# Kernel optimization log

Measured on AMD Instinct MI355X. Metric: run time of the kernel, lower is better.

Reference implementation:

```python
import jax, jax.numpy as jnp
import numpy as np

N_NODES = 40000
N_EDGES = 640000
IN_DIM, H_DIM, OUT_DIM = 128, 128, 64


def setup_inputs() -> dict:
    key = jax.random.key(0)
    ks = jax.random.split(key, 16)
    x = jax.random.normal(ks[0], (N_NODES, IN_DIM), dtype=jnp.float32)
    edge_index = jax.random.randint(ks[1], (2, N_EDGES), 0, N_NODES, dtype=jnp.int64)
    dims = [(IN_DIM, H_DIM), (H_DIM, H_DIM), (H_DIM, OUT_DIM)]
    inp = {"x": x, "edge_index": edge_index}
    for l, (di, do) in enumerate(dims):
        s = 1.0 / np.sqrt(di)
        inp[f"Wr{l}"] = jax.random.uniform(ks[2 + 3 * l], (di, do), jnp.float32, -s, s)  # lin_rel weight
        inp[f"br{l}"] = jax.random.uniform(ks[3 + 3 * l], (do,), jnp.float32, -s, s)     # lin_rel bias
        inp[f"Ws{l}"] = jax.random.uniform(ks[4 + 3 * l], (di, do), jnp.float32, -s, s)  # lin_root weight (no bias)
    return inp


def _graph_conv(x, src, dst, Wr, br, Ws):
    # PyG GraphConv (aggr='add'): out = lin_rel(sum_{j in N(i)} x_j) + lin_root(x_i)
    agg = jax.ops.segment_sum(x[src], dst, num_segments=N_NODES)  # [N, d_in]
    return agg @ Wr + br + x @ Ws


def reference(x, edge_index, Wr0, br0, Ws0, Wr1, br1, Ws1, Wr2, br2, Ws2):
    src, dst = edge_index[0], edge_index[1]
    h = x
    for Wr, br, Ws in ((Wr0, br0, Ws0), (Wr1, br1, Ws1), (Wr2, br2, Ws2)):
        h = _graph_conv(h, src, dst, Wr, br, Ws)
        h = jax.nn.relu(h)
        # dropout p=0 / eval mode -> identity
    return jax.nn.log_softmax(h, axis=1)
```

## Files before the change

kernel.cpp:

```cpp
#include <hip/hip_runtime.h>
#include <hip/hip_bf16.h>


#define N_NODES 40000
#define N_EDGES 640000
#define PAD_NODES 40064
#define DEG_CAP   40960
#define ROW_CAP   64

typedef float v4f __attribute__((ext_vector_type(4)));
typedef float v2f __attribute__((ext_vector_type(2)));
typedef short short8 __attribute__((ext_vector_type(8)));

__device__ inline unsigned short f2b(float f) {
    unsigned u = __float_as_uint(f);
    return (unsigned short)((u + 0x7fffu + ((u >> 16) & 1u)) >> 16);
}

__device__ inline unsigned b2f8(unsigned short us) {
    unsigned s  = ((unsigned)us >> 8) & 0x80u;
    unsigned mag = us & 0x7fffu;
    unsigned e8 = mag >> 7, m7 = mag & 0x7fu;
    unsigned out;
    if (e8 < 121u) out = 0u;
    else if (e8 > 135u) out = 0x7eu;
    else {
        unsigned e4 = e8 - 120u;
        unsigned r  = (m7 + 7u + ((m7 >> 4) & 1u)) >> 4;
        if (r == 8u) { r = 0u; e4++; }
        out = (e4 > 15u || (e4 == 15u && r > 6u)) ? 0x7eu : ((e4 << 3) | r);
    }
    return s | out;
}

__device__ inline unsigned pack4_fp8(float f0, float f1, float f2, float f3) {
#if __has_builtin(__builtin_amdgcn_cvt_pk_fp8_f32)
    int w = __builtin_amdgcn_cvt_pk_fp8_f32(f0, f1, 0, false);
    w = __builtin_amdgcn_cvt_pk_fp8_f32(f2, f3, w, true);
    return (unsigned)w;
#else
    return b2f8(f2b(f0)) | (b2f8(f2b(f1)) << 8) |
           (b2f8(f2b(f2)) << 16) | (b2f8(f2b(f3)) << 24);
#endif
}

#if __has_builtin(__builtin_amdgcn_cvt_f32_fp8)
#define F8TOF(w, sel) __builtin_amdgcn_cvt_f32_fp8((int)(w), (sel))
#else
__device__ inline float f8tof_(unsigned b) {
    unsigned e = (b >> 3) & 15u;
    unsigned bits = ((b & 0x80u) << 24) |
                    (e ? (((e + 120u) << 23) | ((b & 7u) << 20)) : 0u);
    return __uint_as_float(bits);
}
#define F8TOF(w, sel) f8tof_(((unsigned)(w) >> ((sel) * 8)) & 0xffu)
#endif

__device__ inline void addp(v2f* a, uint4 q) {
    v2f t0 = { __uint_as_float(q.x << 16), __uint_as_float(q.x & 0xffff0000u) };
    v2f t1 = { __uint_as_float(q.y << 16), __uint_as_float(q.y & 0xffff0000u) };
    v2f t2 = { __uint_as_float(q.z << 16), __uint_as_float(q.z & 0xffff0000u) };
    v2f t3 = { __uint_as_float(q.w << 16), __uint_as_float(q.w & 0xffff0000u) };
    a[0] += t0; a[1] += t1; a[2] += t2; a[3] += t3;
}
__device__ inline void addp8w(v2f* a, unsigned w) {
    v2f t0 = { F8TOF(w, 0), F8TOF(w, 1) };
    v2f t1 = { F8TOF(w, 2), F8TOF(w, 3) };
    a[0] += t0; a[1] += t1;
}
__device__ inline void addp16(v2f* a, uint4 q) {
    addp8w(a + 0, q.x); addp8w(a + 2, q.y);
    addp8w(a + 4, q.z); addp8w(a + 6, q.w);
}

__global__ __launch_bounds__(256) void prep_kernel(const float* __restrict__ Wr0, const float* __restrict__ Ws0,
                                                   const float* __restrict__ Wr1, const float* __restrict__ Ws1,
                                                   const float* __restrict__ Wr2, const float* __restrict__ Ws2,
                                                   const float* __restrict__ x,
                                                   unsigned short* __restrict__ Wt0,
                                                   unsigned short* __restrict__ Wt1,
                                                   unsigned short* __restrict__ Wt2,
                                                   unsigned short* __restrict__ Xb,
                                                   int* __restrict__ deg) {
    int tid = blockIdx.x * 256 + threadIdx.x;
    if (tid < DEG_CAP / 4) {
        ((int4*)deg)[tid] = make_int4(0, 0, 0, 0);
        return;
    }
    int t = tid - DEG_CAP / 4;
    if (t < 32768) {
        int n = t >> 7, k = t & 127;
        const float* W = (n < 128) ? Wr0 : Ws0;
        Wt0[t] = f2b(W[k * 128 + (n & 127)]);
    } else if (t < 65536) {
        int u = t - 32768;
        int n = u >> 7, k = u & 127;
        const float* W = (n < 128) ? Wr1 : Ws1;
        Wt1[u] = f2b(W[k * 128 + (n & 127)]);
    } else if (t < 81920) {
        int u = t - 65536;
        int n = u >> 7, k = u & 127;
        const float* W = (n < 64) ? Wr2 : Ws2;
        Wt2[u] = f2b(W[k * 64 + (n & 63)]);
    } else {
        int u = t - 81920;
        if (u < (N_NODES * 128) / 8) {
            float4 a = ((const float4*)x)[u * 2];
            float4 b = ((const float4*)x)[u * 2 + 1];
            uint4 o;
            o.x = (unsigned)f2b(a.x) | ((unsigned)f2b(a.y) << 16);
            o.y = (unsigned)f2b(a.z) | ((unsigned)f2b(a.w) << 16);
            o.z = (unsigned)f2b(b.x) | ((unsigned)f2b(b.y) << 16);
            o.w = (unsigned)f2b(b.z) | ((unsigned)f2b(b.w) << 16);
            ((uint4*)Xb)[u] = o;
        }
    }
}

__global__ __launch_bounds__(256) void place_kernel(const int* __restrict__ src,
                                                    const int* __restrict__ dst,
                                                    int* __restrict__ deg,
                                                    int* __restrict__ esrc) {
    int e = blockIdx.x * 256 + threadIdx.x;
    if (e < N_EDGES) {
        int d = dst[e];
        int r = atomicAdd(&deg[d], 1);
        if (r < ROW_CAP) esrc[(size_t)d * ROW_CAP + r] = src[e];
    }
}

template <int DO, bool AGG>
__global__ __launch_bounds__(256, 3) void mmf_kernel(const void* __restrict__ Ain,
                                                     const unsigned short* __restrict__ Sprev,
                                                     const float* __restrict__ brp,
                                                     const int* __restrict__ deg,
                                                     const int* __restrict__ esrc,
                                                     const unsigned short* __restrict__ Wt,
                                                     void* __restrict__ Tout,
                                                     unsigned short* __restrict__ Sout) {
    constexpr int NB  = 2 * DO;
    constexpr int NBW = NB / 4;
    constexpr int CF  = NBW / 16;

    __shared__ unsigned short AsMem[64 * 128];
    __shared__ unsigned short BsMem[NB * 64];
    uint4* As4 = (uint4*)AsMem;
    uint4* Bs4 = (uint4*)BsMem;

    const int tid  = threadIdx.x;
    const int m0   = blockIdx.x * 64;
    const int wave = tid >> 6;
    const int lane = tid & 63;
    const int qm   = lane & 15;
    const int hi   = lane >> 4;
    const int wcb  = wave * NBW;

#pragma unroll
    for (int i = 0; i < NB * 8 / 256; i++) {
        int idx = i * 256 + tid;
        int row = idx >> 3, c8 = idx & 7;
        Bs4[row * 8 + (c8 ^ (row & 7))] =
            *(const uint4*)(Wt + (size_t)row * 128 + c8 * 8);
    }

    if (AGG) {
        const int noderow = tid >> 2;
        const int lane4   = tid & 3;
        const int n       = m0 + noderow;
        if (n < N_NODES) {
            int cnt = deg[n];
            if (cnt > ROW_CAP) cnt = ROW_CAP;
            const int* erow = esrc + (size_t)n * ROW_CAP;
            const uint4* T8 = (const uint4*)Ain;
            v2f acc[16];
#pragma unroll
            for (int i = 0; i < 16; i++) acc[i] = (v2f)(0.0f);
            for (int o = 0; o < cnt; o += 4) {
                int4 i0 = *(const int4*)(erow + o);
                i0.x = (o + 0 < cnt) ? i0.x : N_NODES;
                i0.y = (o + 1 < cnt) ? i0.y : N_NODES;
                i0.z = (o + 2 < cnt) ? i0.z : N_NODES;
                i0.w = (o + 3 < cnt) ? i0.w : N_NODES;
                size_t b0 = (size_t)i0.x * 8 + lane4 * 2;
                size_t b1 = (size_t)i0.y * 8 + lane4 * 2;
                size_t b2 = (size_t)i0.z * 8 + lane4 * 2;
                size_t b3 = (size_t)i0.w * 8 + lane4 * 2;
                uint4 qa0 = T8[b0], qb0 = T8[b0 + 1];
                uint4 qa1 = T8[b1], qb1 = T8[b1 + 1];
                uint4 qa2 = T8[b2], qb2 = T8[b2 + 1];
                uint4 qa3 = T8[b3], qb3 = T8[b3 + 1];
                addp16(acc, qa0); addp16(acc + 8, qb0);
                addp16(acc, qa1); addp16(acc + 8, qb1);
                addp16(acc, qa2); addp16(acc + 8, qb2);
                addp16(acc, qa3); addp16(acc + 8, qb3);
            }
#pragma unroll
            for (int h = 0; h < 4; h++) {
                uint4 sv = ((const uint4*)Sprev)[(size_t)n * 16 + lane4 * 4 + h];
                addp(acc + h * 4, sv);
            }
#pragma unroll
            for (int h = 0; h < 4; h++) {
                float vv[8];
#pragma unroll
                for (int j = 0; j < 8; j++) {
                    int d = h * 8 + j;
                    float bj = brp[lane4 * 32 + d];
                    vv[j] = fmaxf(((d & 1) ? acc[d >> 1].y : acc[d >> 1].x) + bj, 0.f);
                }
                uint4 o;
                o.x = (unsigned)f2b(vv[0]) | ((unsigned)f2b(vv[1]) << 16);
                o.y = (unsigned)f2b(vv[2]) | ((unsigned)f2b(vv[3]) << 16);
                o.z = (unsigned)f2b(vv[4]) | ((unsigned)f2b(vv[5]) << 16);
                o.w = (unsigned)f2b(vv[6]) | ((unsigned)f2b(vv[7]) << 16);
                As4[noderow * 16 + ((lane4 * 4 + h) ^ (noderow & 7))] = o;
            }
        } else {
            uint4 z = make_uint4(0, 0, 0, 0);
#pragma unroll
            for (int h = 0; h < 4; h++)
                As4[noderow * 16 + ((lane4 * 4 + h) ^ (noderow & 7))] = z;
        }
    } else {
        const unsigned short* Ab = (const unsigned short*)Ain;
#pragma unroll
        for (int i = 0; i < 4; i++) {
            int idx = i * 256 + tid;
            int row = idx >> 4, c = idx & 15;
            int gr = m0 + row;
            if (gr > N_NODES - 1) gr = N_NODES - 1;
            As4[row * 16 + (c ^ (row & 7))] =
                *(const uint4*)(Ab + (size_t)gr * 128 + c * 8);
        }
    }
    __syncthreads();

    v4f acc[4][CF];
#pragma unroll
    for (int i = 0; i < 4; i++)
#pragma unroll
        for (int j = 0; j < CF; j++) acc[i][j] = (v4f)(0.0f);

#pragma unroll
    for (int half = 0; half < 2; half++) {
        if (half == 1) {
            __syncthreads();
#pragma unroll
            for (int i = 0; i < NB * 8 / 256; i++) {
                int idx = i * 256 + tid;
                int row = idx >> 3, c8 = idx & 7;
                Bs4[row * 8 + (c8 ^ (row & 7))] =
                    *(const uint4*)(Wt + (size_t)row * 128 + 64 + c8 * 8);
            }
            __syncthreads();
        }
#pragma unroll
        for (int ks = 0; ks < 2; ks++) {
            short8 af[4], bf[CF];
#pragma unroll
            for (int mi = 0; mi < 4; mi++) {
                const int r  = mi * 16 + qm;
                const int ca = half * 8 + ks * 4 + hi;
                af[mi] = *(const short8*)&As4[r * 16 + (ca ^ (r & 7))];
            }
#pragma unroll
            for (int ni = 0; ni < CF; ni++) {
                const int rb = wcb + ni * 16 + qm;
                const int cb = ks * 4 + hi;
                bf[ni] = *(const short8*)&Bs4[rb * 8 + (cb ^ (rb & 7))];
            }
#pragma unroll
            for (int mi = 0; mi < 4; mi++)
#pragma unroll
                for (int ni = 0; ni < CF; ni++)
                    acc[mi][ni] = __builtin_amdgcn_mfma_f32_16x16x32_bf16(af[mi], bf[ni], acc[mi][ni], 0, 0, 0);
        }
    }
    __syncthreads();

    unsigned short* Es = BsMem;
#pragma unroll
    for (int mi = 0; mi < 4; mi++) {
        const int rowBase = mi * 16 + (hi << 2);
#pragma unroll
        for (int r = 0; r < 4; r++) {
            const int row = rowBase + r;
            const int sw  = ((row >> 2) & 3) << 4;
#pragma unroll
            for (int ni = 0; ni < CF; ni++) {
                const int c = wcb + ni * 16 + qm;
                Es[row * NB + (c ^ sw)] = f2b(acc[mi][ni][r]);
            }
        }
    }
    __syncthreads();

    if (DO == 128) {
        unsigned char* T8o = (unsigned char*)Tout;
#pragma unroll
        for (int i = 0; i < 2; i++) {
            const int chunk = i * 256 + tid;
            const int row   = chunk >> 3;
            const int c0    = (chunk & 7) * 16;
            const int sw    = ((row >> 2) & 3) << 4;
            const int node  = m0 + row;
            if (node <= N_NODES) {
                uint4 v = make_uint4(0, 0, 0, 0);
                if (node < N_NODES) {
                    const unsigned short* p = Es + row * 256 + (c0 ^ sw);
                    uint4 ha = *(const uint4*)p;
                    uint4 hb = *(const uint4*)(p + 8);
#define LOF(d) __uint_as_float((d) << 16)
#define HIF(d) __uint_as_float((d) & 0xffff0000u)
                    v.x = pack4_fp8(LOF(ha.x), HIF(ha.x), LOF(ha.y), HIF(ha.y));
                    v.y = pack4_fp8(LOF(ha.z), HIF(ha.z), LOF(ha.w), HIF(ha.w));
                    v.z = pack4_fp8(LOF(hb.x), HIF(hb.x), LOF(hb.y), HIF(hb.y));
                    v.w = pack4_fp8(LOF(hb.z), HIF(hb.z), LOF(hb.w), HIF(hb.w));
#undef LOF
#undef HIF
                }
                *(uint4*)(T8o + (size_t)node * 128 + c0) = v;
            }
        }
#pragma unroll
        for (int i = 0; i < 4; i++) {
            const int chunk = i * 256 + tid;
            const int row   = chunk >> 4;
            const int c0    = 128 + (chunk & 15) * 8;
            const int sw    = ((row >> 2) & 3) << 4;
            const int node  = m0 + row;
            if (node <= N_NODES) {
                uint4 v = make_uint4(0, 0, 0, 0);
                if (node < N_NODES)
                    v = *(const uint4*)(Es + row * 256 + (c0 ^ sw));
                *(uint4*)(Sout + (size_t)node * 128 + (c0 - 128)) = v;
            }
        }
    } else {
        unsigned short* Tb = (unsigned short*)Tout;
#pragma unroll
        for (int i = 0; i < 4; i++) {
            const int chunk = i * 256 + tid;
            const int row   = chunk >> 4;
            const int c0    = (chunk & 15) * 8;
            const int sw    = ((row >> 2) & 3) << 4;
            const int node  = m0 + row;
            if (node <= N_NODES) {
                uint4 v = make_uint4(0, 0, 0, 0);
                if (node < N_NODES)
                    v = *(const uint4*)(Es + row * 128 + (c0 ^ sw));
                if (c0 < 64) *(uint4*)(Tb + (size_t)node * 64 + c0) = v;
                else         *(uint4*)(Sout + (size_t)node * 64 + (c0 - 64)) = v;
            }
        }
    }
}

__global__ __launch_bounds__(256) void agg_last_kernel(const unsigned short* __restrict__ T,
                                                       const unsigned short* __restrict__ S,
                                                       const float* __restrict__ br,
                                                       const int* __restrict__ deg,
                                                       const int* __restrict__ esrc,
                                                       float* __restrict__ Fout) {
    const int lane16 = threadIdx.x & 15;
    const int g      = lane16 >> 3;
    const int lane   = lane16 & 7;
    const int n      = blockIdx.x * 16 + (threadIdx.x >> 4);

    int cnt = deg[n];
    if (cnt > ROW_CAP) cnt = ROW_CAP;
    const int* erow = esrc + (size_t)n * ROW_CAP;
    const uint4* T4 = (const uint4*)T;

    v2f acc[4];
    acc[0] = (v2f)(0.0f); acc[1] = (v2f)(0.0f);
    acc[2] = (v2f)(0.0f); acc[3] = (v2f)(0.0f);

    for (int o = g * 8; o < cnt; o += 16) {
        int4 i0 = *(const int4*)(erow + o);
        int4 i1 = *(const int4*)(erow + o + 4);
        i0.x = (o + 0 < cnt) ? i0.x : N_NODES;
        i0.y = (o + 1 < cnt) ? i0.y : N_NODES;
        i0.z = (o + 2 < cnt) ? i0.z : N_NODES;
        i0.w = (o + 3 < cnt) ? i0.w : N_NODES;
        i1.x = (o + 4 < cnt) ? i1.x : N_NODES;
        i1.y = (o + 5 < cnt) ? i1.y : N_NODES;
        i1.z = (o + 6 < cnt) ? i1.z : N_NODES;
        i1.w = (o + 7 < cnt) ? i1.w : N_NODES;
        uint4 q0 = T4[(size_t)i0.x * 8 + lane];
        uint4 q1 = T4[(size_t)i0.y * 8 + lane];
        uint4 q2 = T4[(size_t)i0.z * 8 + lane];
        uint4 q3 = T4[(size_t)i0.w * 8 + lane];
        uint4 q4 = T4[(size_t)i1.x * 8 + lane];
        uint4 q5 = T4[(size_t)i1.y * 8 + lane];
        uint4 q6 = T4[(size_t)i1.z * 8 + lane];
        uint4 q7 = T4[(size_t)i1.w * 8 + lane];
        addp(acc, q0); addp(acc, q1); addp(acc, q2); addp(acc, q3);
        addp(acc, q4); addp(acc, q5); addp(acc, q6); addp(acc, q7);
    }
#pragma unroll
    for (int i = 0; i < 4; i++) {
        acc[i].x += __shfl_xor(acc[i].x, 8);
        acc[i].y += __shfl_xor(acc[i].y, 8);
    }

    uint4 sv = ((const uint4*)S)[(size_t)n * 8 + lane];
    addp(acc, sv);
    const float4 b0 = ((const float4*)br)[lane * 2];
    const float4 b1 = ((const float4*)br)[lane * 2 + 1];

    float v[8];
    v[0] = fmaxf(acc[0].x + b0.x, 0.f); v[1] = fmaxf(acc[0].y + b0.y, 0.f);
    v[2] = fmaxf(acc[1].x + b0.z, 0.f); v[3] = fmaxf(acc[1].y + b0.w, 0.f);
    v[4] = fmaxf(acc[2].x + b1.x, 0.f); v[5] = fmaxf(acc[2].y + b1.y, 0.f);
    v[6] = fmaxf(acc[3].x + b1.z, 0.f); v[7] = fmaxf(acc[3].y + b1.w, 0.f);

    float m = v[0];
#pragma unroll
    for (int i = 1; i < 8; i++) m = fmaxf(m, v[i]);
#pragma unroll
    for (int off = 4; off; off >>= 1) m = fmaxf(m, __shfl_xor(m, off));
    float es = 0.f;
#pragma unroll
    for (int i = 0; i < 8; i++) es += expf(v[i] - m);
#pragma unroll
    for (int off = 4; off; off >>= 1) es += __shfl_xor(es, off);
    float lse = m + logf(es);
    if (g == 0) {
        float4 o0 = make_float4(v[0] - lse, v[1] - lse, v[2] - lse, v[3] - lse);
        float4 o1 = make_float4(v[4] - lse, v[5] - lse, v[6] - lse, v[7] - lse);
        ((float4*)Fout)[(size_t)n * 16 + lane * 2]     = o0;
        ((float4*)Fout)[(size_t)n * 16 + lane * 2 + 1] = o1;
    }
}


extern "C" void kernel_launch(void* const* d_in, const int* in_sizes, int n_in,
                              void* d_out, int out_size, void* d_ws, size_t ws_size,
                              hipStream_t stream) {
    const float* x    = (const float*)d_in[0];
    const int*   eidx = (const int*)d_in[1];
    const float* Wr0  = (const float*)d_in[2];
    const float* br0  = (const float*)d_in[3];
    const float* Ws0  = (const float*)d_in[4];
    const float* Wr1  = (const float*)d_in[5];
    const float* br1  = (const float*)d_in[6];
    const float* Ws1  = (const float*)d_in[7];
    const float* Wr2  = (const float*)d_in[8];
    const float* br2  = (const float*)d_in[9];
    const float* Ws2  = (const float*)d_in[10];
    float* out = (float*)d_out;

    const int* src = eidx;
    const int* dst = eidx + N_EDGES;

    auto align = [](size_t v) { return (v + 255) & ~(size_t)255; };
    char* w = (char*)d_ws;
    int* deg  = (int*)w;  w += align(sizeof(int) * DEG_CAP);
    int* esrc = (int*)w;  w += align(sizeof(int) * (size_t)N_NODES * ROW_CAP);
    unsigned short* Xb  = (unsigned short*)w;  w += align(2ull * PAD_NODES * 128);
    unsigned short* Wt0 = (unsigned short*)w;  w += align(2ull * 256 * 128);
    unsigned short* Wt1 = (unsigned short*)w;  w += align(2ull * 256 * 128);
    unsigned short* Wt2 = (unsigned short*)w;  w += align(2ull * 128 * 128);
    void* T_a = (void*)w;                      w += align(2ull * PAD_NODES * 64);
    void* T_b = (void*)w;                      w += align(2ull * PAD_NODES * 64);
    unsigned short* S_a = (unsigned short*)w;  w += align(2ull * PAD_NODES * 128);
    unsigned short* S_b = (unsigned short*)w;  w += align(2ull * PAD_NODES * 128);
    (void)ws_size; (void)n_in; (void)in_sizes; (void)out_size;

    prep_kernel<<<(DEG_CAP / 4 + 81920 + (N_NODES * 128) / 8 + 255) / 256, 256, 0, stream>>>(
        Wr0, Ws0, Wr1, Ws1, Wr2, Ws2, x, Wt0, Wt1, Wt2, Xb, deg);

    place_kernel<<<(N_EDGES + 255) / 256, 256, 0, stream>>>(src, dst, deg, esrc);

    mmf_kernel<128, false><<<PAD_NODES / 64, 256, 0, stream>>>(
        Xb, nullptr, nullptr, nullptr, nullptr, Wt0, T_a, S_a);

    mmf_kernel<128, true><<<PAD_NODES / 64, 256, 0, stream>>>(
        T_a, S_a, br0, deg, esrc, Wt1, T_b, S_b);

    mmf_kernel<64, true><<<PAD_NODES / 64, 256, 0, stream>>>(
        T_b, S_b, br1, deg, esrc, Wt2, T_a, S_a);

    agg_last_kernel<<<N_NODES / 16, 256, 0, stream>>>(
        (const unsigned short*)T_a, S_a, br2, deg, esrc, out);
}
```

Measured before the change: 193.0 us.

## Fuse x bf16 conversion into first GEMM, merge prep with edge placement, halve tile rows

Drops the separate x-to-bf16 pass by converting fp32 x in the first mmf kernel's load stage. It merges weight transposition with the edge-placement kernel and zeroes degrees with a memset. Node tiles shrink from 64 to 32 rows, giving twice as many blocks, and aggregation uses 8 lanes per node with 8 neighbours in flight. Weight tile loads move after the A-tile gather. Smaller tiles mean the B weights are reloaded per block more often, and the first layer now reads fp32 x directly.

```diff
diff --git a/kernel.cpp b/kernel.cpp
--- a/kernel.cpp
+++ b/kernel.cpp
@@ -73,63 +73,45 @@
     addp8w(a + 4, q.z); addp8w(a + 6, q.w);
 }
 
-__global__ __launch_bounds__(256) void prep_kernel(const float* __restrict__ Wr0, const float* __restrict__ Ws0,
-                                                   const float* __restrict__ Wr1, const float* __restrict__ Ws1,
-                                                   const float* __restrict__ Wr2, const float* __restrict__ Ws2,
-                                                   const float* __restrict__ x,
-                                                   unsigned short* __restrict__ Wt0,
-                                                   unsigned short* __restrict__ Wt1,
-                                                   unsigned short* __restrict__ Wt2,
-                                                   unsigned short* __restrict__ Xb,
-                                                   int* __restrict__ deg) {
-    int tid = blockIdx.x * 256 + threadIdx.x;
-    if (tid < DEG_CAP / 4) {
-        ((int4*)deg)[tid] = make_int4(0, 0, 0, 0);
-        return;
-    }
-    int t = tid - DEG_CAP / 4;
-    if (t < 32768) {
-        int n = t >> 7, k = t & 127;
-        const float* W = (n < 128) ? Wr0 : Ws0;
-        Wt0[t] = f2b(W[k * 128 + (n & 127)]);
-    } else if (t < 65536) {
-        int u = t - 32768;
-        int n = u >> 7, k = u & 127;
-        const float* W = (n < 128) ? Wr1 : Ws1;
-        Wt1[u] = f2b(W[k * 128 + (n & 127)]);
-    } else if (t < 81920) {
-        int u = t - 65536;
-        int n = u >> 7, k = u & 127;
-        const float* W = (n < 64) ? Wr2 : Ws2;
-        Wt2[u] = f2b(W[k * 64 + (n & 63)]);
+__global__ __launch_bounds__(256) void prep_place_kernel(const int* __restrict__ src,
+                                                         const int* __restrict__ dst,
+                                                         int* __restrict__ deg,
+                                                         int* __restrict__ esrc,
+                                                         const float* __restrict__ Wr0, const float* __restrict__ Ws0,
+                                                         const float* __restrict__ Wr1, const float* __restrict__ Ws1,
+                                                         const float* __restrict__ Wr2, const float* __restrict__ Ws2,
+                                                         unsigned short* __restrict__ Wt0,
+                                                         unsigned short* __restrict__ Wt1,
+                                                         unsigned short* __restrict__ Wt2) {
+    const int bid = blockIdx.x;
+    if (bid < 2500) {
+        int e = bid * 256 + threadIdx.x;
+        if (e < N_EDGES) {
+            int d = dst[e];
+            int r = atomicAdd(&deg[d], 1);
+            if (r < ROW_CAP) esrc[(size_t)d * ROW_CAP + r] = src[e];
+        }
     } else {
-        int u = t - 81920;
-        if (u < (N_NODES * 128) / 8) {
-            float4 a = ((const float4*)x)[u * 2];
-            float4 b = ((const float4*)x)[u * 2 + 1];
-            uint4 o;
-            o.x = (unsigned)f2b(a.x) | ((unsigned)f2b(a.y) << 16);
-            o.y = (unsigned)f2b(a.z) | ((unsigned)f2b(a.w) << 16);
-            o.z = (unsigned)f2b(b.x) | ((unsigned)f2b(b.y) << 16);
-            o.w = (unsigned)f2b(b.z) | ((unsigned)f2b(b.w) << 16);
-            ((uint4*)Xb)[u] = o;
-        }
-    }
-}
-
-__global__ __launch_bounds__(256) void place_kernel(const int* __restrict__ src,
-                                                    const int* __restrict__ dst,
-                                                    int* __restrict__ deg,
-                                                    int* __restrict__ esrc) {
-    int e = blockIdx.x * 256 + threadIdx.x;
-    if (e < N_EDGES) {
-        int d = dst[e];
-        int r = atomicAdd(&deg[d], 1);
-        if (r < ROW_CAP) esrc[(size_t)d * ROW_CAP + r] = src[e];
-    }
-}
-
-template <int DO, bool AGG>
+        int t = (bid - 2500) * 256 + threadIdx.x;
+        if (t < 32768) {
+            int n = t >> 7, k = t & 127;
+            const float* W = (n < 128) ? Wr0 : Ws0;
+            Wt0[t] = f2b(W[k * 128 + (n & 127)]);
+        } else if (t < 65536) {
+            int u = t - 32768;
+            int n = u >> 7, k = u & 127;
+            const float* W = (n < 128) ? Wr1 : Ws1;
+            Wt1[u] = f2b(W[k * 128 + (n & 127)]);
+        } else if (t < 81920) {
+            int u = t - 65536;
+            int n = u >> 7, k = u & 127;
+            const float* W = (n < 64) ? Wr2 : Ws2;
+            Wt2[u] = f2b(W[k * 64 + (n & 63)]);
+        }
+    }
+}
+
+template <int DO, bool AGG, bool F32>
 __global__ __launch_bounds__(256, 3) void mmf_kernel(const void* __restrict__ Ain,
                                                      const unsigned short* __restrict__ Sprev,
                                                      const float* __restrict__ brp,
@@ -142,89 +124,98 @@
     constexpr int NBW = NB / 4;
     constexpr int CF  = NBW / 16;
 
-    __shared__ unsigned short AsMem[64 * 128];
+    __shared__ unsigned short AsMem[32 * 128];
     __shared__ unsigned short BsMem[NB * 64];
     uint4* As4 = (uint4*)AsMem;
     uint4* Bs4 = (uint4*)BsMem;
 
     const int tid  = threadIdx.x;
-    const int m0   = blockIdx.x * 64;
+    const int m0   = blockIdx.x * 32;
     const int wave = tid >> 6;
     const int lane = tid & 63;
     const int qm   = lane & 15;
     const int hi   = lane >> 4;
     const int wcb  = wave * NBW;
 
-#pragma unroll
-    for (int i = 0; i < NB * 8 / 256; i++) {
-        int idx = i * 256 + tid;
-        int row = idx >> 3, c8 = idx & 7;
-        Bs4[row * 8 + (c8 ^ (row & 7))] =
-            *(const uint4*)(Wt + (size_t)row * 128 + c8 * 8);
-    }
-
     if (AGG) {
-        const int noderow = tid >> 2;
-        const int lane4   = tid & 3;
+        const int noderow = tid >> 3;
+        const int lane8   = tid & 7;
         const int n       = m0 + noderow;
         if (n < N_NODES) {
             int cnt = deg[n];
             if (cnt > ROW_CAP) cnt = ROW_CAP;
             const int* erow = esrc + (size_t)n * ROW_CAP;
             const uint4* T8 = (const uint4*)Ain;
-            v2f acc[16];
-#pragma unroll
-            for (int i = 0; i < 16; i++) acc[i] = (v2f)(0.0f);
-            for (int o = 0; o < cnt; o += 4) {
+            v2f acc[8];
+#pragma unroll
+            for (int i = 0; i < 8; i++) acc[i] = (v2f)(0.0f);
+            for (int o = 0; o < cnt; o += 8) {
                 int4 i0 = *(const int4*)(erow + o);
+                int4 i1 = *(const int4*)(erow + o + 4);
                 i0.x = (o + 0 < cnt) ? i0.x : N_NODES;
                 i0.y = (o + 1 < cnt) ? i0.y : N_NODES;
                 i0.z = (o + 2 < cnt) ? i0.z : N_NODES;
                 i0.w = (o + 3 < cnt) ? i0.w : N_NODES;
-                size_t b0 = (size_t)i0.x * 8 + lane4 * 2;
-                size_t b1 = (size_t)i0.y * 8 + lane4 * 2;
-                size_t b2 = (size_t)i0.z * 8 + lane4 * 2;
-                size_t b3 = (size_t)i0.w * 8 + lane4 * 2;
-                uint4 qa0 = T8[b0], qb0 = T8[b0 + 1];
-                uint4 qa1 = T8[b1], qb1 = T8[b1 + 1];
-                uint4 qa2 = T8[b2], qb2 = T8[b2 + 1];
-                uint4 qa3 = T8[b3], qb3 = T8[b3 + 1];
-                addp16(acc, qa0); addp16(acc + 8, qb0);
-                addp16(acc, qa1); addp16(acc + 8, qb1);
-                addp16(acc, qa2); addp16(acc + 8, qb2);
-                addp16(acc, qa3); addp16(acc + 8, qb3);
-            }
-#pragma unroll
-            for (int h = 0; h < 4; h++) {
-                uint4 sv = ((const uint4*)Sprev)[(size_t)n * 16 + lane4 * 4 + h];
-                addp(acc + h * 4, sv);
-            }
-#pragma unroll
-            for (int h = 0; h < 4; h++) {
-                float vv[8];
-#pragma unroll
-                for (int j = 0; j < 8; j++) {
-                    int d = h * 8 + j;
-                    float bj = brp[lane4 * 32 + d];
-                    vv[j] = fmaxf(((d & 1) ? acc[d >> 1].y : acc[d >> 1].x) + bj, 0.f);
-                }
+                i1.x = (o + 4 < cnt) ? i1.x : N_NODES;
+                i1.y = (o + 5 < cnt) ? i1.y : N_NODES;
+                i1.z = (o + 6 < cnt) ? i1.z : N_NODES;
+                i1.w = (o + 7 < cnt) ? i1.w : N_NODES;
+                uint4 q0 = T8[(size_t)i0.x * 8 + lane8];
+                uint4 q1 = T8[(size_t)i0.y * 8 + lane8];
+                uint4 q2 = T8[(size_t)i0.z * 8 + lane8];
+                uint4 q3 = T8[(size_t)i0.w * 8 + lane8];
+                uint4 q4 = T8[(size_t)i1.x * 8 + lane8];
+                uint4 q5 = T8[(size_t)i1.y * 8 + lane8];
+                uint4 q6 = T8[(size_t)i1.z * 8 + lane8];
+                uint4 q7 = T8[(size_t)i1.w * 8 + lane8];
+                addp16(acc, q0); addp16(acc, q1); addp16(acc, q2); addp16(acc, q3);
+                addp16(acc, q4); addp16(acc, q5); addp16(acc, q6); addp16(acc, q7);
+            }
+            uint4 sv0 = ((const uint4*)Sprev)[(size_t)n * 16 + lane8 * 2];
+            uint4 sv1 = ((const uint4*)Sprev)[(size_t)n * 16 + lane8 * 2 + 1];
+            addp(acc, sv0); addp(acc + 4, sv1);
+            float vv[16];
+#pragma unroll
+            for (int j = 0; j < 16; j++) {
+                float bj = brp[lane8 * 16 + j];
+                vv[j] = fmaxf(((j & 1) ? acc[j >> 1].y : acc[j >> 1].x) + bj, 0.f);
+            }
+#pragma unroll
+            for (int h = 0; h < 2; h++) {
                 uint4 o;
-                o.x = (unsigned)f2b(vv[0]) | ((unsigned)f2b(vv[1]) << 16);
-                o.y = (unsigned)f2b(vv[2]) | ((unsigned)f2b(vv[3]) << 16);
-                o.z = (unsigned)f2b(vv[4]) | ((unsigned)f2b(vv[5]) << 16);
-                o.w = (unsigned)f2b(vv[6]) | ((unsigned)f2b(vv[7]) << 16);
-                As4[noderow * 16 + ((lane4 * 4 + h) ^ (noderow & 7))] = o;
+                o.x = (unsigned)f2b(vv[h * 8 + 0]) | ((unsigned)f2b(vv[h * 8 + 1]) << 16);
+                o.y = (unsigned)f2b(vv[h * 8 + 2]) | ((unsigned)f2b(vv[h * 8 + 3]) << 16);
+                o.z = (unsigned)f2b(vv[h * 8 + 4]) | ((unsigned)f2b(vv[h * 8 + 5]) << 16);
+                o.w = (unsigned)f2b(vv[h * 8 + 6]) | ((unsigned)f2b(vv[h * 8 + 7]) << 16);
+                As4[noderow * 16 + ((lane8 * 2 + h) ^ (noderow & 7))] = o;
             }
         } else {
             uint4 z = make_uint4(0, 0, 0, 0);
 #pragma unroll
-            for (int h = 0; h < 4; h++)
-                As4[noderow * 16 + ((lane4 * 4 + h) ^ (noderow & 7))] = z;
+            for (int h = 0; h < 2; h++)
+                As4[noderow * 16 + ((lane8 * 2 + h) ^ (noderow & 7))] = z;
+        }
+    } else if (F32) {
+        const float4* Xg = (const float4*)Ain;
+#pragma unroll
+        for (int i = 0; i < 2; i++) {
+            int idx = i * 256 + tid;
+            int row = idx >> 4, c = idx & 15;
+            int gr = m0 + row;
+            if (gr > N_NODES - 1) gr = N_NODES - 1;
+            float4 a = Xg[(size_t)gr * 32 + c * 2];
+            float4 b = Xg[(size_t)gr * 32 + c * 2 + 1];
+            uint4 o;
+            o.x = (unsigned)f2b(a.x) | ((unsigned)f2b(a.y) << 16);
+            o.y = (unsigned)f2b(a.z) | ((unsigned)f2b(a.w) << 16);
+            o.z = (unsigned)f2b(b.x) | ((unsigned)f2b(b.y) << 16);
+            o.w = (unsigned)f2b(b.z) | ((unsigned)f2b(b.w) << 16);
+            As4[row * 16 + (c ^ (row & 7))] = o;
         }
     } else {
         const unsigned short* Ab = (const unsigned short*)Ain;
 #pragma unroll
-        for (int i = 0; i < 4; i++) {
+        for (int i = 0; i < 2; i++) {
             int idx = i * 256 + tid;
             int row = idx >> 4, c = idx & 15;
             int gr = m0 + row;
@@ -233,11 +224,19 @@
                 *(const uint4*)(Ab + (size_t)gr * 128 + c * 8);
         }
     }
+
+#pragma unroll
+    for (int i = 0; i < NB * 8 / 256; i++) {
+        int idx = i * 256 + tid;
+        int row = idx >> 3, c8 = idx & 7;
+        Bs4[row * 8 + (c8 ^ (row & 7))] =
+            *(const uint4*)(Wt + (size_t)row * 128 + c8 * 8);
+    }
     __syncthreads();
 
-    v4f acc[4][CF];
-#pragma unroll
-    for (int i = 0; i < 4; i++)
+    v4f acc[2][CF];
+#pragma unroll
+    for (int i = 0; i < 2; i++)
 #pragma unroll
         for (int j = 0; j < CF; j++) acc[i][j] = (v4f)(0.0f);
 
@@ -256,9 +255,9 @@
         }
 #pragma unroll
         for (int ks = 0; ks < 2; ks++) {
-            short8 af[4], bf[CF];
-#pragma unroll
-            for (int mi = 0; mi < 4; mi++) {
+            short8 af[2], bf[CF];
+#pragma unroll
+            for (int mi = 0; mi < 2; mi++) {
                 const int r  = mi * 16 + qm;
                 const int ca = half * 8 + ks * 4 + hi;
                 af[mi] = *(const short8*)&As4[r * 16 + (ca ^ (r & 7))];
@@ -270,7 +269,7 @@
                 bf[ni] = *(const short8*)&Bs4[rb * 8 + (cb ^ (rb & 7))];
             }
 #pragma unroll
-            for (int mi = 0; mi < 4; mi++)
+            for (int mi = 0; mi < 2; mi++)
 #pragma unroll
                 for (int ni = 0; ni < CF; ni++)
                     acc[mi][ni] = __builtin_amdgcn_mfma_f32_16x16x32_bf16(af[mi], bf[ni], acc[mi][ni], 0, 0, 0);
@@ -280,7 +279,7 @@
 
     unsigned short* Es = BsMem;
 #pragma unroll
-    for (int mi = 0; mi < 4; mi++) {
+    for (int mi = 0; mi < 2; mi++) {
         const int rowBase = mi * 16 + (hi << 2);
 #pragma unroll
         for (int r = 0; r < 4; r++) {
@@ -297,9 +296,8 @@
 
     if (DO == 128) {
         unsigned char* T8o = (unsigned char*)Tout;
-#pragma unroll
-        for (int i = 0; i < 2; i++) {
-            const int chunk = i * 256 + tid;
+        {
+            const int chunk = tid;
             const int row   = chunk >> 3;
             const int c0    = (chunk & 7) * 16;
             const int sw    = ((row >> 2) & 3) << 4;
@@ -323,7 +321,7 @@
             }
         }
 #pragma unroll
-        for (int i = 0; i < 4; i++) {
+        for (int i = 0; i < 2; i++) {
             const int chunk = i * 256 + tid;
             const int row   = chunk >> 4;
             const int c0    = 128 + (chunk & 15) * 8;
@@ -339,7 +337,7 @@
     } else {
         unsigned short* Tb = (unsigned short*)Tout;
 #pragma unroll
-        for (int i = 0; i < 4; i++) {
+        for (int i = 0; i < 2; i++) {
             const int chunk = i * 256 + tid;
             const int row   = chunk >> 4;
             const int c0    = (chunk & 15) * 8;
@@ -458,7 +456,6 @@
     char* w = (char*)d_ws;
     int* deg  = (int*)w;  w += align(sizeof(int) * DEG_CAP);
     int* esrc = (int*)w;  w += align(sizeof(int) * (size_t)N_NODES * ROW_CAP);
-    unsigned short* Xb  = (unsigned short*)w;  w += align(2ull * PAD_NODES * 128);
     unsigned short* Wt0 = (unsigned short*)w;  w += align(2ull * 256 * 128);
     unsigned short* Wt1 = (unsigned short*)w;  w += align(2ull * 256 * 128);
     unsigned short* Wt2 = (unsigned short*)w;  w += align(2ull * 128 * 128);
@@ -468,18 +465,17 @@
     unsigned short* S_b = (unsigned short*)w;  w += align(2ull * PAD_NODES * 128);
     (void)ws_size; (void)n_in; (void)in_sizes; (void)out_size;
 
-    prep_kernel<<<(DEG_CAP / 4 + 81920 + (N_NODES * 128) / 8 + 255) / 256, 256, 0, stream>>>(
-        Wr0, Ws0, Wr1, Ws1, Wr2, Ws2, x, Wt0, Wt1, Wt2, Xb, deg);
-
-    place_kernel<<<(N_EDGES + 255) / 256, 256, 0, stream>>>(src, dst, deg, esrc);
-
-    mmf_kernel<128, false><<<PAD_NODES / 64, 256, 0, stream>>>(
-        Xb, nullptr, nullptr, nullptr, nullptr, Wt0, T_a, S_a);
-
-    mmf_kernel<128, true><<<PAD_NODES / 64, 256, 0, stream>>>(
+    hipMemsetAsync(deg, 0, sizeof(int) * DEG_CAP, stream);
+    prep_place_kernel<<<2820, 256, 0, stream>>>(
+        src, dst, deg, esrc, Wr0, Ws0, Wr1, Ws1, Wr2, Ws2, Wt0, Wt1, Wt2);
+
+    mmf_kernel<128, false, true><<<PAD_NODES / 32, 256, 0, stream>>>(
+        x, nullptr, nullptr, nullptr, nullptr, Wt0, T_a, S_a);
+
+    mmf_kernel<128, true, false><<<PAD_NODES / 32, 256, 0, stream>>>(
         T_a, S_a, br0, deg, esrc, Wt1, T_b, S_b);
 
-    mmf_kernel<64, true><<<PAD_NODES / 64, 256, 0, stream>>>(
+    mmf_kernel<64, true, false><<<PAD_NODES / 32, 256, 0, stream>>>(
         T_b, S_b, br1, deg, esrc, Wt2, T_a, S_a);
 
     agg_last_kernel<<<N_NODES / 16, 256, 0, stream>>>(
```

Result: faster. 185.0 us (-4.1%).
